# Kernel optimization log

Measured on AMD Instinct MI355X. Metric: run time of the kernel, lower is better.

The kernel has to match this reference:

```python
import jax, jax.numpy as jnp
import numpy as np

N = 8192          # num atoms
APM = 32          # atoms per molecule
M = N // APM      # 256 molecules
FEAT = 100        # hidden_channels == num_filters
NG = 25           # num gaussians
K = 28            # knn neighbors
L = 4             # num interaction blocks
CUTOFF = 6.0
LOG2 = float(np.log(2.0))


def ssp(x):
    # pyg ShiftedSoftplus: softplus(x) - log(2)
    return jax.nn.softplus(x) - LOG2


def setup_inputs() -> dict:
    key = jax.random.key(0)
    ks = jax.random.split(key, 16)
    z = jax.random.randint(ks[0], (N,), 1, 100)
    pos = jax.random.normal(ks[1], (N, 3), jnp.float32) * 2.0
    ptr = jnp.arange(0, N + APM, APM)  # [M+1] molecule boundaries

    def w(k, shape, fan):
        return (jax.random.normal(k, shape, jnp.float32) / np.sqrt(fan)).astype(jnp.float32)

    def b(k, shape):
        return jax.random.normal(k, shape, jnp.float32) * 0.01

    kb = jax.random.split(ks[15], 8)
    H = FEAT // 2
    return {
        "z": z,
        "pos": pos,
        "ptr": ptr,
        "emb": jax.random.normal(ks[2], (100, FEAT), jnp.float32),
        "mlp_w1": w(ks[3], (L, NG, FEAT), NG),
        "mlp_b1": b(kb[0], (L, FEAT)),
        "mlp_w2": w(ks[4], (L, FEAT, FEAT), FEAT),
        "mlp_b2": b(kb[1], (L, FEAT)),
        "lin1_w": w(ks[5], (L, FEAT, FEAT), FEAT),
        "lin2_w": w(ks[6], (L, FEAT, FEAT), FEAT),
        "lin2_b": b(kb[2], (L, FEAT)),
        "lin_w": w(ks[7], (L, FEAT, FEAT), FEAT),
        "lin_b": b(kb[3], (L, FEAT)),
        "out_w1": w(ks[8], (FEAT, H), FEAT),
        "out_b1": b(kb[4], (H,)),
        "out_w2": w(ks[9], (H, 1), H),
        "out_b2": b(kb[5], (1,)),
    }


def reference(z, pos, ptr, emb, mlp_w1, mlp_b1, mlp_w2, mlp_b2,
              lin1_w, lin2_w, lin2_b, lin_w, lin_b,
              out_w1, out_b1, out_w2, out_b2):
    n = z.shape[0]
    m = ptr.shape[0] - 1

    # ptr -> per-atom batch ids (index_fill + cumsum; OOB index N dropped)
    flag = jnp.zeros((n,), jnp.int32).at[ptr].set(1, mode="drop")
    flag = flag.at[0].set(0)
    batch = jnp.cumsum(flag)

    # ---- KNN interaction graph (full NxN pairwise distances + masking + topk)
    diff = pos[:, None, :] - pos[None, :, :]           # [N,N,3]
    d2 = jnp.sum(diff * diff, axis=-1)                  # [N,N]
    ar = jnp.arange(n)
    mask = (ar[:, None] == ar[None, :]) \
         | (batch[:, None] != batch[None, :]) \
         | (d2 > CUTOFF * CUTOFF)
    dist = jnp.where(mask, CUTOFF, jnp.sqrt(jnp.where(mask, 1.0, d2)))
    neg, idx = jax.lax.top_k(-dist, K)                  # k nearest per row
    ew = -neg.reshape(-1)                               # edge distances [N*K]
    src = idx.reshape(-1)                               # source atoms j; target of edge (i,m) is i

    # ---- Gaussian smearing
    offset = jnp.linspace(0.0, CUTOFF, NG)
    coeff = -0.5 / (offset[1] - offset[0]) ** 2
    ea = jnp.exp(coeff * (ew[:, None] - offset[None, :]) ** 2)  # [E,NG]

    # cosine cutoff (zero weight for padded edges at dist==cutoff)
    ccut = 0.5 * (jnp.cos(ew * jnp.pi / CUTOFF) + 1.0)          # [E]

    h = emb[z]                                                   # [N,F]
    f = h.shape[1]
    for l in range(L):
        # filter network on edge attributes
        Wf = ssp(ea @ mlp_w1[l] + mlp_b1[l]) @ mlp_w2[l] + mlp_b2[l]
        Wf = Wf * ccut[:, None]                                  # [E,F]
        # CFConv: lin1 -> gather*filter -> sum over k neighbors -> lin2
        x1 = h @ lin1_w[l]                                       # [N,F]
        msg = x1[src] * Wf                                       # [E,F]
        agg = msg.reshape(n, K, f).sum(axis=1)                   # each node i has exactly K incoming edges
        v = ssp(agg @ lin2_w[l] + lin2_b[l]) @ lin_w[l] + lin_b[l]
        h = h + v

    # readout head
    h = ssp(h @ out_w1 + out_b1)
    per_atom = (h @ out_w2 + out_b2).reshape(-1)                 # [N]
    return jax.ops.segment_sum(per_atom, batch, num_segments=m) # per-molecule energy [M]
```

## Files before the change

### kernel.cpp

```cpp
#include <hip/hip_runtime.h>
#include <math.h>

#define APM   32
#define NMOL  256
#define FEAT  100
#define NPAD  112
#define LAYERS 4
#define NTHREADS 1024
#define NWAVES   16
#define G_TBL 1024
#define TSTR  128
#define X1STR 132

typedef _Float16 f16x8 __attribute__((ext_vector_type(8)));
typedef float    f32x4 __attribute__((ext_vector_type(4)));

#define L1F_OFF 0
#define L2F_OFF 14336
#define LVF_OFF 28672
#define LWTOT   43008
#define WTOTAL  (4*LWTOT)

#define PREP_BLOCKS 672
#define TBL_BLOCKS  128

__device__ __forceinline__ float sspf(float x){
  return __logf(1.0f + __expf(x)) - 0.69314718056f;
}

__global__ __launch_bounds__(256) void prep_all(
    const float* __restrict__ lin1_w, const float* __restrict__ lin2_w,
    const float* __restrict__ lin_w,
    const float* __restrict__ mlp_w1, const float* __restrict__ mlp_b1,
    const float* __restrict__ mlp_w2, const float* __restrict__ mlp_b2,
    _Float16* __restrict__ outw, float* __restrict__ tbl)
{
  if (blockIdx.x < PREP_BLOCKS){
    int gid = blockIdx.x*256 + threadIdx.x;
    int l = gid / LWTOT;
    int r = gid - l*LWTOT;
    const float* W; int e;
    if (r < 14336)      { W = lin1_w + l*10000; e = r; }
    else if (r < 28672) { W = lin2_w + l*10000; e = r - 14336; }
    else                { W = lin_w  + l*10000; e = r - 28672; }
    int j = e & 7, L = (e >> 3) & 63, tile = e >> 9;
    int kc = tile / 7, nt = tile - kc*7;
    int k = kc*32 + ((L >> 4) << 3) + j;
    int f = nt*16 + (L & 15);
    float v = (k < 100 && f < FEAT) ? W[k*FEAT + f] : 0.0f;
    outw[gid] = (_Float16)v;
    return;
  }
  __shared__ float sW2[10000];
  __shared__ float sW1[2500];
  __shared__ float sB1[100], sB2[100];
  __shared__ float sT[4][100];
  int bid = blockIdx.x - PREP_BLOCKS;
  int l = bid >> 5;
  int s0 = (bid & 31) * 32;
  int tid = threadIdx.x, wv = tid >> 6, lane = tid & 63;
  for (int i = tid; i < 10000; i += 256) sW2[i] = mlp_w2[l*10000 + i];
  for (int i = tid; i < 2500;  i += 256) sW1[i] = mlp_w1[l*2500 + i];
  if (tid < 100) sB1[tid] = mlp_b1[l*100 + tid];
  if (tid >= 128 && tid < 228) sB2[tid-128] = mlp_b2[l*100 + tid-128];
  __syncthreads();
  #pragma unroll 1
  for (int si = 0; si < 8; si++){
    int s = s0 + wv*8 + si;
    float d = 6.0f * (float)s / (float)(G_TBL - 1);
    float ea[25];
    #pragma unroll
    for (int g = 0; g < 25; g++){
      float u = d - 0.25f*(float)g;
      ea[g] = __expf(-8.0f*u*u);
    }
    #pragma unroll
    for (int kk = 0; kk < 2; kk++){
      int k = lane + kk*64;
      if (k < 100){
        float acc = sB1[k];
        #pragma unroll
        for (int g = 0; g < 25; g++)
          acc += ea[g] * sW1[g*100 + k];
        sT[wv][k] = sspf(acc);
      }
    }
    float cc = 0.5f*(__cosf(d*0.52359877559f) + 1.0f);
    #pragma unroll
    for (int ff = 0; ff < 2; ff++){
      int f = lane + ff*64;
      float o = 0.0f;
      if (f < 100){
        o = sB2[f];
        for (int k = 0; k < 100; k++)
          o += sT[wv][k] * sW2[k*100 + f];
        o *= cc;
      }
      tbl[((size_t)l*G_TBL + s)*TSTR + f] = o;
    }
  }
}

__global__ __launch_bounds__(1024)
__attribute__((amdgpu_waves_per_eu(4, 4)))
void schnet_mega(
    const int* __restrict__ z, const float* __restrict__ pos,
    const float* __restrict__ emb, const _Float16* __restrict__ wf,
    const float* __restrict__ tbl,
    const float* __restrict__ lin2_b, const float* __restrict__ lin_b,
    const float* __restrict__ out_w1, const float* __restrict__ out_b1,
    const float* __restrict__ out_w2, const float* __restrict__ out_b2,
    float* __restrict__ out)
{
  __shared__ __align__(16) _Float16 sAf[APM*136];
  __shared__ __align__(16) _Float16 sBf[APM*136];
  __shared__ __align__(16) float    sX1[APM*X1STR];
  __shared__ __align__(16) float    sH [APM*NPAD];
  __shared__ float sD  [APM*33];
  __shared__ int   sOff[APM*33];
  __shared__ float sFr [APM*33];
  __shared__ float sPos[96];
  __shared__ float sPart[NWAVES];

  int tid = threadIdx.x, lane = tid & 63, wv = tid >> 6;
  int q = lane >> 4, n = lane & 15;
  int mol = blockIdx.x, mb = mol*APM;

  if (tid < 96) sPos[tid] = pos[mb*3 + tid];
  if (tid < 512){
    int r0 = tid >> 4, c0 = 112 + (tid & 15);
    sBf[r0*136 + c0] = (_Float16)0.0f;
  }
  for (int i = tid; i < APM*20; i += NTHREADS){
    int r = i/20, c = 112 + (i - r*20);
    sX1[r*X1STR + c] = 0.0f;
  }
  for (int i = tid; i < APM*136; i += NTHREADS){
    int r = i/136, c = i - r*136;
    float v = (c < FEAT) ? emb[z[mb+r]*FEAT + c] : 0.0f;
    sAf[i] = (_Float16)v;
    if (c < NPAD) sH[r*NPAD + c] = v;
  }
  __syncthreads();
  for (int p = tid; p < APM*APM; p += NTHREADS){
    int i = p >> 5, j = p & 31;
    float dx = sPos[i*3+0]-sPos[j*3+0];
    float dy = sPos[i*3+1]-sPos[j*3+1];
    float dz = sPos[i*3+2]-sPos[j*3+2];
    float d2 = dx*dx + dy*dy + dz*dz;
    sD[i*33+j] = (d2 > 36.0f) ? 6.0f : sqrtf(d2);
  }
  __syncthreads();
  if (tid < APM){
    float dd[32];
    #pragma unroll
    for (int j = 0; j < 32; j++) dd[j] = sD[tid*33+j];
    dd[tid] = 1e30f;
    unsigned dropped = 0u;
    for (int rr = 0; rr < 4; rr++){
      float mx = -1.0f; int mj = 0;
      #pragma unroll
      for (int j = 0; j < 32; j++){
        bool ok = !((dropped>>j)&1u) && (dd[j] > mx);
        mx = ok ? dd[j] : mx;  mj = ok ? j : mj;
      }
      dropped |= 1u << mj;
    }
    #pragma unroll
    for (int j = 0; j < 32; j++){
      float d = ((dropped>>j)&1u) ? 6.0f : dd[j];
      float un = d * (float)((G_TBL-1)/6.0);
      int s = (int)un;
      s = (s > G_TBL-2) ? (G_TBL-2) : s;
      sOff[tid*33+j] = s*TSTR;
      sFr [tid*33+j] = un - (float)s;
    }
  }
  __syncthreads();

  for (int l = 0; l < LAYERS; l++){
    const _Float16* w1b = wf + l*LWTOT + L1F_OFF;
    const _Float16* w2b = wf + l*LWTOT + L2F_OFF;
    const _Float16* wvb = wf + l*LWTOT + LVF_OFF;
    const float* tb = tbl + (size_t)l*G_TBL*TSTR;
    for (int tau = wv; tau < 14; tau += NWAVES){
      int mt = tau/7, nt = tau - mt*7;
      f32x4 acc = {0.0f,0.0f,0.0f,0.0f};
      #pragma unroll
      for (int kc = 0; kc < 4; kc++){
        f16x8 av = *(const f16x8*)&sAf[(mt*16+n)*136 + kc*32 + q*8];
        f16x8 bv = *(const f16x8*)&w1b[((kc*7+nt)*64 + lane)*8];
        acc = __builtin_amdgcn_mfma_f32_16x16x32_f16(av, bv, acc, 0, 0, 0);
      }
      #pragma unroll
      for (int r = 0; r < 4; r++)
        sX1[(mt*16+q*4+r)*X1STR + nt*16+n] = acc[r];
    }
    __syncthreads();
    {
      int half = lane >> 5, L = lane & 31;
      int a = wv*2 + half, arow = a*33;
      float ag0=0.0f, ag1=0.0f, ag2=0.0f, ag3=0.0f;
      f32x4 A0[4], A1[4]; float fA[4];
      f32x4 B0[4], B1[4]; float fB[4];

#define GLD(J0, V0, V1, FR)                                            \
      { _Pragma("unroll")                                              \
        for (int u = 0; u < 4; u++){                                   \
          const float* r0 = tb + (sOff[arow + (J0) + u] + L);          \
          FR[u] = sFr[arow + (J0) + u];                                \
          V0[u][0] = r0[0];       V0[u][1] = r0[32];                   \
          V0[u][2] = r0[64];      V0[u][3] = r0[96];                   \
          V1[u][0] = r0[TSTR];    V1[u][1] = r0[TSTR+32];              \
          V1[u][2] = r0[TSTR+64]; V1[u][3] = r0[TSTR+96];              \
        } }
#define GCMP(J0, V0, V1, FR)                                           \
      { _Pragma("unroll")                                              \
        for (int u = 0; u < 4; u++){                                   \
          const float* xp = &sX1[((J0)+u)*X1STR + L];                  \
          f32x4 wl_ = V0[u] + FR[u]*(V1[u] - V0[u]);                   \
          ag0 += wl_[0]*xp[0];  ag1 += wl_[1]*xp[32];                  \
          ag2 += wl_[2]*xp[64]; ag3 += wl_[3]*xp[96];                  \
        } }

      GLD(0, A0, A1, fA)
      #pragma unroll
      for (int b = 0; b < 8; b += 2){
        GLD((b+1)*4, B0, B1, fB)
        GCMP(b*4, A0, A1, fA)
        if (b+2 < 8) GLD((b+2)*4, A0, A1, fA)
        GCMP((b+1)*4, B0, B1, fB)
      }
#undef GLD
#undef GCMP
      int ab = a*136 + L;
      sAf[ab]    = (_Float16)ag0;
      sAf[ab+32] = (_Float16)ag1;
      sAf[ab+64] = (_Float16)ag2;
      sAf[ab+96] = (_Float16)ag3;
    }
    __syncthreads();
    for (int tau = wv; tau < 14; tau += NWAVES){
      int mt = tau/7, nt = tau - mt*7;
      f32x4 acc = {0.0f,0.0f,0.0f,0.0f};
      #pragma unroll
      for (int kc = 0; kc < 4; kc++){
        f16x8 av = *(const f16x8*)&sAf[(mt*16+n)*136 + kc*32 + q*8];
        f16x8 bv = *(const f16x8*)&w2b[((kc*7+nt)*64 + lane)*8];
        acc = __builtin_amdgcn_mfma_f32_16x16x32_f16(av, bv, acc, 0, 0, 0);
      }
      int f = nt*16 + n;
      float bb = (f < FEAT) ? lin2_b[l*FEAT + f] : 0.0f;
      #pragma unroll
      for (int r = 0; r < 4; r++)
        sBf[(mt*16+q*4+r)*136 + f] = (_Float16)sspf(acc[r] + bb);
    }
    __syncthreads();
    for (int tau = wv; tau < 14; tau += NWAVES){
      int mt = tau/7, nt = tau - mt*7;
      f32x4 acc = {0.0f,0.0f,0.0f,0.0f};
      #pragma unroll
      for (int kc = 0; kc < 4; kc++){
        f16x8 av = *(const f16x8*)&sBf[(mt*16+n)*136 + kc*32 + q*8];
        f16x8 bv = *(const f16x8*)&wvb[((kc*7+nt)*64 + lane)*8];
        acc = __builtin_amdgcn_mfma_f32_16x16x32_f16(av, bv, acc, 0, 0, 0);
      }
      int f = nt*16 + n;
      if (f < FEAT){
        float bb = lin_b[l*FEAT + f];
        #pragma unroll
        for (int r = 0; r < 4; r++){
          int row = mt*16 + q*4 + r;
          float hn = sH[row*NPAD + f] + acc[r] + bb;
          sH[row*NPAD + f] = hn;
          sAf[row*136 + f] = (_Float16)hn;
        }
      }
    }
    __syncthreads();
  }

  float ob2 = out_b2[0];
  float partial = 0.0f;
  for (int t = 0; t < 2; t++){
    int a = wv*2 + t;
    float u = 0.0f;
    if (lane < 50){
      u = out_b1[lane];
      #pragma unroll 4
      for (int c = 0; c < FEAT; c++)
        u += sH[a*NPAD + c] * out_w1[c*50 + lane];
      u = sspf(u) * out_w2[lane];
    }
    #pragma unroll
    for (int s = 1; s < 64; s <<= 1) u += __shfl_xor(u, s);
    partial += u + ob2;
  }
  if (lane == 0) sPart[wv] = partial;
  __syncthreads();
  if (tid == 0){
    float s = 0.0f;
    #pragma unroll
    for (int i = 0; i < NWAVES; i++) s += sPart[i];
    out[mol] = s;
  }
}

extern "C" void kernel_launch(void* const* d_in, const int* in_sizes, int n_in,
                              void* d_out, int out_size, void* d_ws, size_t ws_size,
                              hipStream_t stream)
{
  const int*   z      = (const int*)  d_in[0];
  const float* pos    = (const float*)d_in[1];
  const float* emb    = (const float*)d_in[3];
  const float* mlp_w1 = (const float*)d_in[4];
  const float* mlp_b1 = (const float*)d_in[5];
  const float* mlp_w2 = (const float*)d_in[6];
  const float* mlp_b2 = (const float*)d_in[7];
  const float* lin1_w = (const float*)d_in[8];
  const float* lin2_w = (const float*)d_in[9];
  const float* lin2_b = (const float*)d_in[10];
  const float* lin_w  = (const float*)d_in[11];
  const float* lin_b  = (const float*)d_in[12];
  const float* out_w1 = (const float*)d_in[13];
  const float* out_b1 = (const float*)d_in[14];
  const float* out_w2 = (const float*)d_in[15];
  const float* out_b2 = (const float*)d_in[16];

  _Float16* wfrag = (_Float16*)d_ws;
  float*    tbl   = (float*)((char*)d_ws + WTOTAL*2);

  prep_all<<<PREP_BLOCKS + TBL_BLOCKS, 256, 0, stream>>>(
      lin1_w, lin2_w, lin_w, mlp_w1, mlp_b1, mlp_w2, mlp_b2, wfrag, tbl);
  schnet_mega<<<NMOL, NTHREADS, 0, stream>>>(z, pos, emb, wfrag, tbl,
      lin2_b, lin_b, out_w1, out_b1, out_w2, out_b2, (float*)d_out);
}
```

Measured before the change: 180.9 us.

## Pack filter table as fp16 pairs and skip dropped edges in aggregation

The precomputed filter lookup table changes from fp32 rows to fp16 pairs holding entries s and s+1 together. Each interpolation then needs one 4-byte gather per feature lane instead of two fp32 loads. The edge list is also compacted to the 28 kept neighbours, with an index array, so the 4 dropped edges per atom are no longer gathered and accumulated. This cuts table gather traffic and loop work, at the cost of fp16 rounding in the filter values and an extra indirection through sJx for the sX1 reads.

```diff
diff --git a/kernel.cpp b/kernel.cpp
--- a/kernel.cpp
+++ b/kernel.cpp
@@ -9,10 +9,12 @@
 #define NTHREADS 1024
 #define NWAVES   16
 #define G_TBL 1024
-#define TSTR  128
+#define PSTR  128
 #define X1STR 132
+#define KEDGE 28
 
 typedef _Float16 f16x8 __attribute__((ext_vector_type(8)));
+typedef _Float16 f16x2 __attribute__((ext_vector_type(2)));
 typedef float    f32x4 __attribute__((ext_vector_type(4)));
 
 #define L1F_OFF 0
@@ -33,7 +35,7 @@
     const float* __restrict__ lin_w,
     const float* __restrict__ mlp_w1, const float* __restrict__ mlp_b1,
     const float* __restrict__ mlp_w2, const float* __restrict__ mlp_b2,
-    _Float16* __restrict__ outw, float* __restrict__ tbl)
+    _Float16* __restrict__ outw, f16x2* __restrict__ tblp)
 {
   if (blockIdx.x < PREP_BLOCKS){
     int gid = blockIdx.x*256 + threadIdx.x;
@@ -55,6 +57,7 @@
   __shared__ float sW1[2500];
   __shared__ float sB1[100], sB2[100];
   __shared__ float sT[4][100];
+  __shared__ float sV[33][128];
   int bid = blockIdx.x - PREP_BLOCKS;
   int l = bid >> 5;
   int s0 = (bid & 31) * 32;
@@ -63,10 +66,15 @@
   for (int i = tid; i < 2500;  i += 256) sW1[i] = mlp_w1[l*2500 + i];
   if (tid < 100) sB1[tid] = mlp_b1[l*100 + tid];
   if (tid >= 128 && tid < 228) sB2[tid-128] = mlp_b2[l*100 + tid-128];
+  if (tid < 128){ sV[32][tid] = 0.0f; }
+  for (int i = tid; i < 33*128; i += 256)
+    ((float*)sV)[i] = 0.0f;
   __syncthreads();
   #pragma unroll 1
-  for (int si = 0; si < 8; si++){
-    int s = s0 + wv*8 + si;
+  for (int si = 0; si < 9; si++){
+    int li = wv*8 + si;
+    if (li > 32 || (si == 8 && wv != 3)) continue;
+    int s = s0 + li; if (s > G_TBL-1) s = G_TBL-1;
     float d = 6.0f * (float)s / (float)(G_TBL - 1);
     float ea[25];
     #pragma unroll
@@ -89,15 +97,19 @@
     #pragma unroll
     for (int ff = 0; ff < 2; ff++){
       int f = lane + ff*64;
-      float o = 0.0f;
       if (f < 100){
-        o = sB2[f];
+        float o = sB2[f];
         for (int k = 0; k < 100; k++)
           o += sT[wv][k] * sW2[k*100 + f];
-        o *= cc;
-      }
-      tbl[((size_t)l*G_TBL + s)*TSTR + f] = o;
-    }
+        sV[li][f] = o * cc;
+      }
+    }
+  }
+  __syncthreads();
+  for (int i = tid; i < 32*128; i += 256){
+    int s = i >> 7, f = i & 127;
+    f16x2 pr = { (_Float16)sV[s][f], (_Float16)sV[s+1][f] };
+    tblp[((size_t)l*G_TBL + s0 + s)*PSTR + f] = pr;
   }
 }
 
@@ -106,7 +118,7 @@
 void schnet_mega(
     const int* __restrict__ z, const float* __restrict__ pos,
     const float* __restrict__ emb, const _Float16* __restrict__ wf,
-    const float* __restrict__ tbl,
+    const f16x2* __restrict__ tblp,
     const float* __restrict__ lin2_b, const float* __restrict__ lin_b,
     const float* __restrict__ out_w1, const float* __restrict__ out_b1,
     const float* __restrict__ out_w2, const float* __restrict__ out_b2,
@@ -117,8 +129,9 @@
   __shared__ __align__(16) float    sX1[APM*X1STR];
   __shared__ __align__(16) float    sH [APM*NPAD];
   __shared__ float sD  [APM*33];
-  __shared__ int   sOff[APM*33];
-  __shared__ float sFr [APM*33];
+  __shared__ int   sOffC[APM*KEDGE];
+  __shared__ float sFrC [APM*KEDGE];
+  __shared__ int   sJx  [APM*KEDGE];
   __shared__ float sPos[96];
   __shared__ float sPart[NWAVES];
 
@@ -166,14 +179,16 @@
       }
       dropped |= 1u << mj;
     }
-    #pragma unroll
+    int e = 0;
     for (int j = 0; j < 32; j++){
-      float d = ((dropped>>j)&1u) ? 6.0f : dd[j];
-      float un = d * (float)((G_TBL-1)/6.0);
+      if ((dropped>>j)&1u) continue;
+      float un = dd[j] * (float)((G_TBL-1)/6.0);
       int s = (int)un;
       s = (s > G_TBL-2) ? (G_TBL-2) : s;
-      sOff[tid*33+j] = s*TSTR;
-      sFr [tid*33+j] = un - (float)s;
+      sOffC[tid*KEDGE + e] = s*PSTR;
+      sFrC [tid*KEDGE + e] = un - (float)s;
+      sJx  [tid*KEDGE + e] = j;
+      e++;
     }
   }
   __syncthreads();
@@ -182,7 +197,7 @@
     const _Float16* w1b = wf + l*LWTOT + L1F_OFF;
     const _Float16* w2b = wf + l*LWTOT + L2F_OFF;
     const _Float16* wvb = wf + l*LWTOT + LVF_OFF;
-    const float* tb = tbl + (size_t)l*G_TBL*TSTR;
+    const f16x2* tb = tblp + (size_t)l*G_TBL*PSTR;
     for (int tau = wv; tau < 14; tau += NWAVES){
       int mt = tau/7, nt = tau - mt*7;
       f32x4 acc = {0.0f,0.0f,0.0f,0.0f};
@@ -199,37 +214,43 @@
     __syncthreads();
     {
       int half = lane >> 5, L = lane & 31;
-      int a = wv*2 + half, arow = a*33;
+      int a = wv*2 + half, ar = a*KEDGE;
       float ag0=0.0f, ag1=0.0f, ag2=0.0f, ag3=0.0f;
-      f32x4 A0[4], A1[4]; float fA[4];
-      f32x4 B0[4], B1[4]; float fB[4];
-
-#define GLD(J0, V0, V1, FR)                                            \
+      f16x2 PA[4][4]; float fA[4]; int jA[4];
+      f16x2 PB[4][4]; float fB[4]; int jB[4];
+
+#define GLD(E0, P, FR, JV)                                             \
       { _Pragma("unroll")                                              \
         for (int u = 0; u < 4; u++){                                   \
-          const float* r0 = tb + (sOff[arow + (J0) + u] + L);          \
-          FR[u] = sFr[arow + (J0) + u];                                \
-          V0[u][0] = r0[0];       V0[u][1] = r0[32];                   \
-          V0[u][2] = r0[64];      V0[u][3] = r0[96];                   \
-          V1[u][0] = r0[TSTR];    V1[u][1] = r0[TSTR+32];              \
-          V1[u][2] = r0[TSTR+64]; V1[u][3] = r0[TSTR+96];              \
+          int e = ar + (E0) + u;                                       \
+          const f16x2* rp = tb + (sOffC[e] + L);                       \
+          FR[u] = sFrC[e]; JV[u] = sJx[e];                             \
+          P[u][0] = rp[0];  P[u][1] = rp[32];                          \
+          P[u][2] = rp[64]; P[u][3] = rp[96];                          \
         } }
-#define GCMP(J0, V0, V1, FR)                                           \
+#define GCMP(P, FR, JV)                                                \
       { _Pragma("unroll")                                              \
         for (int u = 0; u < 4; u++){                                   \
-          const float* xp = &sX1[((J0)+u)*X1STR + L];                  \
-          f32x4 wl_ = V0[u] + FR[u]*(V1[u] - V0[u]);                   \
-          ag0 += wl_[0]*xp[0];  ag1 += wl_[1]*xp[32];                  \
-          ag2 += wl_[2]*xp[64]; ag3 += wl_[3]*xp[96];                  \
+          const float* xp = &sX1[JV[u]*X1STR + L];                     \
+          float fr = FR[u];                                            \
+          float v0, v1, w_;                                            \
+          v0 = (float)P[u][0].x; v1 = (float)P[u][0].y;                \
+          w_ = v0 + fr*(v1-v0); ag0 += w_*xp[0];                       \
+          v0 = (float)P[u][1].x; v1 = (float)P[u][1].y;                \
+          w_ = v0 + fr*(v1-v0); ag1 += w_*xp[32];                      \
+          v0 = (float)P[u][2].x; v1 = (float)P[u][2].y;                \
+          w_ = v0 + fr*(v1-v0); ag2 += w_*xp[64];                      \
+          v0 = (float)P[u][3].x; v1 = (float)P[u][3].y;                \
+          w_ = v0 + fr*(v1-v0); ag3 += w_*xp[96];                      \
         } }
 
-      GLD(0, A0, A1, fA)
-      #pragma unroll
-      for (int b = 0; b < 8; b += 2){
-        GLD((b+1)*4, B0, B1, fB)
-        GCMP(b*4, A0, A1, fA)
-        if (b+2 < 8) GLD((b+2)*4, A0, A1, fA)
-        GCMP((b+1)*4, B0, B1, fB)
+      GLD(0, PA, fA, jA)
+      #pragma unroll
+      for (int b = 0; b < 7; b += 2){
+        if (b+1 < 7) GLD((b+1)*4, PB, fB, jB)
+        GCMP(PA, fA, jA)
+        if (b+2 < 7) GLD((b+2)*4, PA, fA, jA)
+        if (b+1 < 7) GCMP(PB, fB, jB)
       }
 #undef GLD
 #undef GCMP
@@ -328,10 +349,10 @@
   const float* out_b2 = (const float*)d_in[16];
 
   _Float16* wfrag = (_Float16*)d_ws;
-  float*    tbl   = (float*)((char*)d_ws + WTOTAL*2);
+  f16x2*    tblp  = (f16x2*)((char*)d_ws + WTOTAL*2);
 
   prep_all<<<PREP_BLOCKS + TBL_BLOCKS, 256, 0, stream>>>(
-      lin1_w, lin2_w, lin_w, mlp_w1, mlp_b1, mlp_w2, mlp_b2, wfrag, tbl);
-  schnet_mega<<<NMOL, NTHREADS, 0, stream>>>(z, pos, emb, wfrag, tbl,
+      lin1_w, lin2_w, lin_w, mlp_w1, mlp_b1, mlp_w2, mlp_b2, wfrag, tblp);
+  schnet_mega<<<NMOL, NTHREADS, 0, stream>>>(z, pos, emb, wfrag, tblp,
       lin2_b, lin_b, out_w1, out_b1, out_w2, out_b2, (float*)d_out);
 }
```

Result: faster. 176.7 us (-2.3%).
